# Optimization experiments

Hardware: AMD Instinct MI355X
Metric: run time of the kernel (lower is better)

## Reference

```python
import math
import jax, jax.numpy as jnp
import numpy as np

NUM_HEADS = 8
FACTOR = 5


def setup_inputs() -> dict:
    key = jax.random.key(0)
    ks = jax.random.split(key, 8)
    B, N, C = 8, 4096, 512
    s = 0.02
    x = jax.random.normal(ks[0], (B, N, C), dtype=jnp.float32)
    Wq = jax.random.normal(ks[1], (C, C), dtype=jnp.float32) * s
    Wk = jax.random.normal(ks[2], (C, C), dtype=jnp.float32) * s
    Wv = jax.random.normal(ks[3], (C, C), dtype=jnp.float32) * s
    Wp = jax.random.normal(ks[4], (C, C), dtype=jnp.float32) * s
    bq = jnp.zeros((C,), jnp.float32)
    bk = jnp.zeros((C,), jnp.float32)
    bv = jnp.zeros((C,), jnp.float32)
    bp = jnp.zeros((C,), jnp.float32)
    sample_k = min(FACTOR * int(np.ceil(np.log(N))), N)  # 45
    index_sample = jax.random.randint(ks[5], (N, sample_k), 0, N, dtype=jnp.int64)
    return {"x": x, "Wq": Wq, "bq": bq, "Wk": Wk, "bk": bk,
            "Wv": Wv, "bv": bv, "Wp": Wp, "bp": bp,
            "index_sample": index_sample}


def reference(x, Wq, bq, Wk, bk, Wv, bv, Wp, bp, index_sample):
    B, N, C = x.shape
    H = NUM_HEADS
    Dh = C // H
    L_Q = L_K = N
    # qkv projections (torch Linear: x @ W.T + b; W sampled symmetric so use x @ W + b)
    q = (x @ Wq + bq).reshape(B, N, H, Dh).transpose(0, 2, 1, 3)  # [B,H,L,Dh]
    k = (x @ Wk + bk).reshape(B, N, H, Dh).transpose(0, 2, 1, 3)
    v = (x @ Wv + bv).reshape(B, N, H, Dh).transpose(0, 2, 1, 3)

    u = min(FACTOR * int(np.ceil(np.log(L_Q))), L_Q)  # n_top
    scale = (C // H) ** (-0.5)

    # _prob_QK: sampled scores per query
    K_sample = k[:, :, index_sample, :]                       # [B,H,L_Q,s,Dh]
    QK_sample = jnp.einsum('bhld,bhlsd->bhls', q, K_sample)   # [B,H,L_Q,s]
    M = QK_sample.max(axis=-1) - QK_sample.sum(axis=-1) / L_K # sparsity measure
    _, M_top = jax.lax.top_k(M, u)                            # [B,H,u]
    Q_reduce = jnp.take_along_axis(q, M_top[..., None], axis=2)  # [B,H,u,Dh]
    scores = jnp.einsum('bhud,bhkd->bhuk', Q_reduce, k) * scale  # [B,H,u,L_K]

    # initial context: mean of V over keys (mask_flag=False)
    context = jnp.broadcast_to(v.mean(axis=2, keepdims=True), (B, H, L_Q, Dh))

    # update context at selected queries
    attn = jax.nn.softmax(scores, axis=-1)
    out_u = jnp.einsum('bhuk,bhkd->bhud', attn, v)            # [B,H,u,Dh]
    bI = jnp.arange(B)[:, None, None]
    hI = jnp.arange(H)[None, :, None]
    context = context.at[bI, hI, M_top].set(out_u)            # [B,H,L_Q,Dh]

    # mix=True: reshape [B,H,N,Dh] -> [B,N,H*Dh] directly (faithful to source)
    context = context.reshape(B, N, H * Dh)
    return context @ Wp + bp
```

## Files before the change

kernel.cpp:

```cpp
#include <hip/hip_runtime.h>
#include <float.h>

typedef unsigned short ushort_t;
typedef short bf16x8 __attribute__((ext_vector_type(8)));
typedef _Float16 f16x8 __attribute__((ext_vector_type(8)));
typedef float f32x4 __attribute__((ext_vector_type(4)));

#define NS 4096
#define ND 64
#define NU 45
#define NUP 48

__device__ __forceinline__ float bf2f(ushort_t u){ return __uint_as_float(((unsigned)u)<<16); }
__device__ __forceinline__ ushort_t f2bf(float f){
  unsigned u = __float_as_uint(f);
  u += 0x7fffu + ((u>>16)&1u);
  return (ushort_t)(u>>16);
}
__device__ __forceinline__ ushort_t f2h(float f){ _Float16 h=(_Float16)f; return __builtin_bit_cast(ushort_t, h); }
__device__ __forceinline__ float h2f(ushort_t u){ return (float)__builtin_bit_cast(_Float16, u); }

__global__ __launch_bounds__(256) void k_wsplit(const float* __restrict__ Wq,
                                                const float* __restrict__ Wk,
                                                const float* __restrict__ Wv,
                                                ushort_t* __restrict__ wh,
                                                ushort_t* __restrict__ wl)
{
  int i = blockIdx.x*256 + threadIdx.x;
  int c = i >> 9, k = i & 511;
  const float* W = (c < 512) ? Wq : (c < 1024 ? Wk : Wv);
  float v = W[k*512 + (c & 511)];
  ushort_t h = f2bf(v);
  wh[i] = h;
  wl[i] = f2bf(v - bf2f(h));
}

__global__ __launch_bounds__(256) void k_gemm_qkv(
    const float* __restrict__ x,
    const ushort_t* __restrict__ wh, const ushort_t* __restrict__ wl,
    const float* __restrict__ bq, const float* __restrict__ bk, const float* __restrict__ bv,
    float* __restrict__ qf, float* __restrict__ kf, ushort_t* __restrict__ vfT,
    ushort_t* __restrict__ kh16)
{
  __shared__ __align__(16) ushort_t Ah[128*40], Al[128*40];
  __shared__ __align__(16) ushort_t Bh[128*40], Bl[128*40];
  const int t = threadIdx.x;
  const int l = t & 63;
  const int w = t >> 6;
  const int wm = w >> 1, wn = w & 1;
  const int rowbase = blockIdx.y * 128;
  const int colbase = blockIdx.x * 128;
  const int mat = colbase >> 9;
  f32x4 acc[4][4] = {};
  const int r0 = t >> 2;
  const int c0 = (t & 3) * 8;

  for (int k0 = 0; k0 < 512; k0 += 32) {
    __syncthreads();
    #pragma unroll
    for (int half = 0; half < 2; half++) {
      const int r = r0 + half*64;
      const float* xp = &x[(size_t)(rowbase + r)*512 + k0 + c0];
      float4 v0 = *(const float4*)xp;
      float4 v1 = *(const float4*)(xp + 4);
      ushort_t hi[8], lo[8];
      float vv[8] = {v0.x,v0.y,v0.z,v0.w,v1.x,v1.y,v1.z,v1.w};
      #pragma unroll
      for (int j = 0; j < 8; j++) {
        hi[j] = f2bf(vv[j]);
        lo[j] = f2bf(vv[j] - bf2f(hi[j]));
      }
      *(uint4*)(&Ah[r*40 + c0]) = *(const uint4*)hi;
      *(uint4*)(&Al[r*40 + c0]) = *(const uint4*)lo;
      *(uint4*)(&Bh[r*40 + c0]) = *(const uint4*)(&wh[(size_t)(colbase + r)*512 + k0 + c0]);
      *(uint4*)(&Bl[r*40 + c0]) = *(const uint4*)(&wl[(size_t)(colbase + r)*512 + k0 + c0]);
    }
    __syncthreads();
    bf16x8 ah[4], al[4], bh8[4], bl8[4];
    #pragma unroll
    for (int m = 0; m < 4; m++) {
      const int off = (wm*64 + m*16 + (l & 15))*40 + (l >> 4)*8;
      ah[m] = *(const bf16x8*)(&Ah[off]);
      al[m] = *(const bf16x8*)(&Al[off]);
    }
    #pragma unroll
    for (int n = 0; n < 4; n++) {
      const int off = (wn*64 + n*16 + (l & 15))*40 + (l >> 4)*8;
      bh8[n] = *(const bf16x8*)(&Bh[off]);
      bl8[n] = *(const bf16x8*)(&Bl[off]);
    }
    #pragma unroll
    for (int m = 0; m < 4; m++)
      #pragma unroll
      for (int n = 0; n < 4; n++) {
        acc[m][n] = __builtin_amdgcn_mfma_f32_16x16x32_bf16(ah[m], bh8[n], acc[m][n], 0, 0, 0);
        acc[m][n] = __builtin_amdgcn_mfma_f32_16x16x32_bf16(ah[m], bl8[n], acc[m][n], 0, 0, 0);
        acc[m][n] = __builtin_amdgcn_mfma_f32_16x16x32_bf16(al[m], bh8[n], acc[m][n], 0, 0, 0);
      }
  }

  const float* bias_p = (mat == 0) ? bq : (mat == 1 ? bk : bv);
  float* dst = (mat == 0) ? qf : kf;
  #pragma unroll
  for (int n = 0; n < 4; n++) {
    const int wi = (colbase & 511) + wn*64 + n*16 + (l & 15);
    const int hh = wi >> 6, d = wi & 63;
    const float bias = bias_p[wi];
    #pragma unroll
    for (int m = 0; m < 4; m++) {
      const int rb = rowbase + wm*64 + m*16 + ((l >> 4) << 2);
      const int b  = rb >> 12, nr = rb & 4095;
      if (mat < 2) {
        #pragma unroll
        for (int j = 0; j < 4; j++) {
          const size_t o = ((size_t)(b*8 + hh)*NS + nr + j)*ND + d;
          const float val = acc[m][n][j] + bias;
          dst[o] = val;
          if (mat == 1 && kh16) kh16[o] = f2h(val);
        }
      } else {
        ushort4 pk;
        pk.x = f2h(acc[m][n][0] + bias);
        pk.y = f2h(acc[m][n][1] + bias);
        pk.z = f2h(acc[m][n][2] + bias);
        pk.w = f2h(acc[m][n][3] + bias);
        *(ushort4*)(&vfT[((size_t)(b*8 + hh)*ND + d)*NS + nr]) = pk;
      }
    }
  }
}

__global__ __launch_bounds__(256) void k_m_approx(const float* __restrict__ qf,
                                                  const ushort_t* __restrict__ kh16,
                                                  const int* __restrict__ idxs,
                                                  float* __restrict__ Mv)
{
  __shared__ float qs[4][64];
  __shared__ int   sidx[4][48];
  const int orig = blockIdx.y * 1024 + blockIdx.x;
  const int lin  = (orig & 7) * 8192 + (orig >> 3);
  const int bh   = lin >> 10;
  const int lc   = lin & 1023;
  const int t = threadIdx.x;
  const int wv = t >> 6, lane = t & 63;
  const int l = lc*4 + wv;
  qs[wv][lane] = qf[((size_t)bh*NS + l)*ND + lane];
  for (int e = t; e < 4*NU; e += 256)
    sidx[e/NU][e%NU] = idxs[(size_t)(lc*4 + e/NU)*NU + e%NU];
  __syncthreads();
  const int g  = lane >> 3;
  const int dq = lane & 7;
  const float* qp = &qs[wv][dq*8];
  float mx = -FLT_MAX, sm = 0.f;
  #pragma unroll
  for (int p = 0; p < 6; p++) {
    const int s = p*8 + g;
    const bool val = (s < NU);
    const int id = sidx[wv][val ? s : NU-1];
    uint4 ku = *(const uint4*)(&kh16[((size_t)bh*NS + id)*ND + dq*8]);
    f16x8 k8 = __builtin_bit_cast(f16x8, ku);
    float p_dot = qp[0]*(float)k8[0] + qp[1]*(float)k8[1] + qp[2]*(float)k8[2] + qp[3]*(float)k8[3]
                + qp[4]*(float)k8[4] + qp[5]*(float)k8[5] + qp[6]*(float)k8[6] + qp[7]*(float)k8[7];
    p_dot += __shfl_xor(p_dot, 1, 64);
    p_dot += __shfl_xor(p_dot, 2, 64);
    p_dot += __shfl_xor(p_dot, 4, 64);
    if (val) { mx = fmaxf(mx, p_dot); sm += p_dot; }
  }
  #pragma unroll
  for (int o = 8; o < 64; o <<= 1) {
    mx = fmaxf(mx, __shfl_xor(mx, o, 64));
    sm += __shfl_xor(sm, o, 64);
  }
  if (lane == 0) Mv[bh*NS + l] = mx - sm * (1.0f/(float)NS);
}

__global__ __launch_bounds__(256) void k_m_exact_full(const float* __restrict__ qf,
                                                      const float* __restrict__ kf,
                                                      const int* __restrict__ idxs,
                                                      float* __restrict__ Mv)
{
  const int bh = blockIdx.y;
  const int l  = blockIdx.x*4 + (threadIdx.x >> 6);
  const int lane = threadIdx.x & 63;
  const int g  = lane >> 2;
  const int dq = lane & 3;
  const float* qrow = qf + ((size_t)bh*NS + l)*ND + dq*16;
  const float4 q0 = *(const float4*)(qrow + 0);
  const float4 q1 = *(const float4*)(qrow + 4);
  const float4 q2 = *(const float4*)(qrow + 8);
  const float4 q3 = *(const float4*)(qrow + 12);
  const float* kbase = kf + (size_t)bh*NS*ND;
  const int* ib = idxs + (size_t)l*NU;
  float mx = -FLT_MAX, sm = 0.f;
  #pragma unroll
  for (int p3 = 0; p3 < 3; p3++) {
    const int s = p3*16 + g;
    const int id = ib[s < NU ? s : NU-1];
    const float* kr = kbase + (size_t)id*ND + dq*16;
    const float4 k0 = *(const float4*)(kr + 0);
    const float4 k1 = *(const float4*)(kr + 4);
    const float4 k2 = *(const float4*)(kr + 8);
    const float4 k3 = *(const float4*)(kr + 12);
    float p = q0.x*k0.x + q0.y*k0.y + q0.z*k0.z + q0.w*k0.w
            + q1.x*k1.x + q1.y*k1.y + q1.z*k1.z + q1.w*k1.w
            + q2.x*k2.x + q2.y*k2.y + q2.z*k2.z + q2.w*k2.w
            + q3.x*k3.x + q3.y*k3.y + q3.z*k3.z + q3.w*k3.w;
    p += __shfl_xor(p, 1, 64);
    p += __shfl_xor(p, 2, 64);
    if (s < NU) { mx = fmaxf(mx, p); sm += p; }
  }
  #pragma unroll
  for (int o = 4; o < 64; o <<= 1) {
    mx = fmaxf(mx, __shfl_xor(mx, o, 64));
    sm += __shfl_xor(sm, o, 64);
  }
  if (lane == 0) Mv[bh*NS + l] = mx - sm * (1.0f/(float)NS);
}

template<int NSEL, int OST>
__global__ __launch_bounds__(256) void k_topk(const float* __restrict__ Mv, int* __restrict__ dst)
{
  __shared__ float wvs[4];
  __shared__ int   wis[4];
  const int bh = blockIdx.x, t = threadIdx.x;
  const int wv = t >> 6, lane = t & 63;
  float v[16];
  #pragma unroll
  for (int j = 0; j < 16; j++) v[j] = Mv[bh*NS + j*256 + t];
  unsigned removed = 0;
  float tmax = -FLT_MAX; int tidx = 0x7fffffff;
  #pragma unroll
  for (int j = 0; j < 16; j++) {
    if (v[j] > tmax) { tmax = v[j]; tidx = j*256 + t; }
  }
  for (int it = 0; it < NSEL; it++) {
    float mv = tmax; int mi = tidx;
    #pragma unroll
    for (int o = 1; o < 64; o <<= 1) {
      float vo = __shfl_xor(mv, o, 64); int io = __shfl_xor(mi, o, 64);
      if (vo > mv || (vo == mv && io < mi)) { mv = vo; mi = io; }
    }
    if (lane == 0) { wvs[wv] = mv; wis[wv] = mi; }
    __syncthreads();
    float gv = wvs[0]; int gi = wis[0];
    #pragma unroll
    for (int k2 = 1; k2 < 4; k2++) {
      float vo = wvs[k2]; int io = wis[k2];
      if (vo > gv || (vo == gv && io < gi)) { gv = vo; gi = io; }
    }
    if (t == 0) dst[bh*OST + it] = gi;
    if ((gi & 255) == t) {
      removed |= 1u << (gi >> 8);
      tmax = -FLT_MAX; tidx = 0x7fffffff;
      #pragma unroll
      for (int j = 0; j < 16; j++) {
        bool ok = ((removed >> j) & 1u) == 0u;
        if (ok && (v[j] > tmax || (v[j] == tmax && (j*256+t) < tidx))) { tmax = v[j]; tidx = j*256 + t; }
      }
    }
    __syncthreads();
  }
}

__global__ __launch_bounds__(256) void k_mexact(const float* __restrict__ qf,
                                                const float* __restrict__ kf,
                                                const int* __restrict__ idxs,
                                                const int* __restrict__ Cand,
                                                float* __restrict__ Mex)
{
  const int bh = blockIdx.y, qtr = blockIdx.x, t = threadIdx.x;
  const int c = qtr*16 + (t >> 4);
  const int dl = t & 15;
  const int l = Cand[bh*64 + c];
  const float4 q4 = *(const float4*)(&qf[((size_t)bh*NS + l)*ND + dl*4]);
  const float* kbase = kf + (size_t)bh*NS*ND;
  const int* ib = idxs + (size_t)l*NU;
  float mx = -FLT_MAX, sm = 0.f;
  for (int s = 0; s < NU; s++) {
    const int id = ib[s];
    const float4 k4 = *(const float4*)(&kbase[(size_t)id*ND + dl*4]);
    float p = q4.x*k4.x + q4.y*k4.y + q4.z*k4.z + q4.w*k4.w;
    p += __shfl_xor(p, 1, 64);
    p += __shfl_xor(p, 2, 64);
    p += __shfl_xor(p, 4, 64);
    p += __shfl_xor(p, 8, 64);
    mx = fmaxf(mx, p);
    sm += p;
  }
  if (dl == 0) Mex[bh*64 + c] = mx - sm * (1.0f/(float)NS);
}

__global__ void k_sel45(const float* __restrict__ Mex, const int* __restrict__ Cand,
                        int* __restrict__ Mtop)
{
  const int bh = blockIdx.x, lane = threadIdx.x;
  float val = Mex[bh*64 + lane];
  const int n = Cand[bh*64 + lane];
  for (int it = 0; it < NU; it++) {
    float wv = val; int wn = n;
    #pragma unroll
    for (int o = 1; o < 64; o <<= 1) {
      float vo = __shfl_xor(wv, o, 64); int io = __shfl_xor(wn, o, 64);
      if (vo > wv || (vo == wv && io < wn)) { wv = vo; wn = io; }
    }
    if (lane == 0) Mtop[bh*NUP + it] = wn;
    if (n == wn) val = -FLT_MAX;
  }
}

__global__ __launch_bounds__(256) void k_qreduce(const float* __restrict__ qf,
                                                 const int* __restrict__ Mtop,
                                                 ushort_t* __restrict__ Qr)
{
  const int bh = blockIdx.x, t = threadIdx.x;
  for (int e = t; e < NUP*ND; e += 256) {
    const int u = e >> 6, d = e & 63;
    float v = 0.f;
    if (u < NU) { const int r = Mtop[bh*NUP + u]; v = qf[((size_t)bh*NS + r)*ND + d]; }
    Qr[bh*NUP*ND + e] = f2bf(v);
  }
}

__global__ __launch_bounds__(256) void k_scores(const ushort_t* __restrict__ Qr,
                                                const float* __restrict__ kf,
                                                ushort_t* __restrict__ scores)
{
  __shared__ __align__(16) ushort_t Ql[NUP*80];
  const int bh = blockIdx.y;
  const int n0 = blockIdx.x * 256;
  const int t = threadIdx.x, w = t >> 6, l = t & 63;
  for (int chunk = t; chunk < NUP*8; chunk += 256) {
    const int r = chunk >> 3, cp = chunk & 7;
    *(uint4*)(&Ql[r*80 + cp*8]) = *(const uint4*)(&Qr[((size_t)bh*NUP + r)*ND + cp*8]);
  }
  __syncthreads();
  f32x4 acc[3][4] = {};
  const float* kbb = kf + (size_t)bh*NS*ND;
  const int nw = n0 + w*64;
  #pragma unroll
  for (int ks = 0; ks < 2; ks++) {
    bf16x8 a[3], b8[4];
    #pragma unroll
    for (int m = 0; m < 3; m++)
      a[m] = *(const bf16x8*)(&Ql[(m*16 + (l & 15))*80 + (l >> 4)*8 + ks*32]);
    #pragma unroll
    for (int n = 0; n < 4; n++) {
      const float* kr = &kbb[(size_t)(nw + n*16 + (l & 15))*ND + (l >> 4)*8 + ks*32];
      float4 u0 = *(const float4*)kr;
      float4 u1 = *(const float4*)(kr + 4);
      ushort_t tmp[8] = {f2bf(u0.x),f2bf(u0.y),f2bf(u0.z),f2bf(u0.w),
                         f2bf(u1.x),f2bf(u1.y),f2bf(u1.z),f2bf(u1.w)};
      b8[n] = *(const bf16x8*)tmp;
    }
    #pragma unroll
    for (int m = 0; m < 3; m++)
      #pragma unroll
      for (int n = 0; n < 4; n++)
        acc[m][n] = __builtin_amdgcn_mfma_f32_16x16x32_bf16(a[m], b8[n], acc[m][n], 0, 0, 0);
  }
  #pragma unroll
  for (int m = 0; m < 3; m++)
    #pragma unroll
    for (int n = 0; n < 4; n++)
      #pragma unroll
      for (int j = 0; j < 4; j++) {
        const int row = m*16 + (l >> 4)*4 + j;
        const int col = nw + n*16 + (l & 15);
        scores[((size_t)bh*NUP + row)*NS + col] = f2bf(acc[m][n][j] * 0.125f);
      }
}

__global__ __launch_bounds__(256) void k_softmax(ushort_t* __restrict__ scores)
{
  __shared__ float srow[NS];
  __shared__ float red[256];
  const int bh = blockIdx.y, u = blockIdx.x, t = threadIdx.x;
  ushort_t* row = scores + ((size_t)bh*NUP + u)*NS;
  float mx = -FLT_MAX;
  for (int j = t; j < NS; j += 256) { float v = bf2f(row[j]); srow[j] = v; mx = fmaxf(mx, v); }
  red[t] = mx; __syncthreads();
  for (int s = 128; s > 0; s >>= 1) { if (t < s) red[t] = fmaxf(red[t], red[t+s]); __syncthreads(); }
  mx = red[0]; __syncthreads();
  float sm = 0.f;
  for (int j = t; j < NS; j += 256) { const float e = __expf(srow[j] - mx); srow[j] = e; sm += e; }
  red[t] = sm; __syncthreads();
  for (int s = 128; s > 0; s >>= 1) { if (t < s) red[t] += red[t+s]; __syncthreads(); }
  const float inv = 1.0f / red[0];
  for (int j = t; j < NS; j += 256) row[j] = f2h(srow[j] * inv);
}

__global__ __launch_bounds__(256) void k_vmean(const ushort_t* __restrict__ vfT, float* __restrict__ vmean)
{
  __shared__ float red[256];
  const int d = blockIdx.x, bh = blockIdx.y, t = threadIdx.x;
  const ushort_t* vr = vfT + ((size_t)bh*ND + d)*NS;
  float s = 0.f;
  for (int n = t; n < NS; n += 256) s += h2f(vr[n]);
  red[t] = s; __syncthreads();
  for (int st = 128; st > 0; st >>= 1) { if (t < st) red[t] += red[t+st]; __syncthreads(); }
  if (t == 0) vmean[bh*ND + d] = red[0] * (1.0f/(float)NS);
}

__global__ __launch_bounds__(256) void k_outu(const ushort_t* __restrict__ attn,
                                              const ushort_t* __restrict__ vfT,
                                              float* __restrict__ pout)
{
  const int bh = blockIdx.y, ch = blockIdx.x;
  const int t = threadIdx.x, w = t >> 6, l = t & 63;
  if (w >= 3) return;
  const ushort_t* ab = attn + (size_t)bh*NUP*NS;
  const ushort_t* vb = vfT + (size_t)bh*ND*NS;
  f32x4 acc[4] = {};
  const int arow = w*16 + (l & 15);
  const int koff = (l >> 4)*8;
  const int kbeg = ch*512;
  for (int kc = kbeg; kc < kbeg + 512; kc += 32) {
    uint4 au = *(const uint4*)(&ab[(size_t)arow*NS + kc + koff]);
    f16x8 a = __builtin_bit_cast(f16x8, au);
    #pragma unroll
    for (int nt = 0; nt < 4; nt++) {
      uint4 bu = *(const uint4*)(&vb[(size_t)(nt*16 + (l & 15))*NS + kc + koff]);
      f16x8 b = __builtin_bit_cast(f16x8, bu);
      acc[nt] = __builtin_amdgcn_mfma_f32_16x16x32_f16(a, b, acc[nt], 0, 0, 0);
    }
  }
  #pragma unroll
  for (int nt = 0; nt < 4; nt++)
    #pragma unroll
    for (int j = 0; j < 4; j++) {
      const int u = w*16 + (l >> 4)*4 + j;
      const int d = nt*16 + (l & 15);
      pout[(((size_t)bh*8 + ch)*NUP + u)*ND + d] = acc[nt][j];
    }
}

__global__ __launch_bounds__(256) void k_delta_fin(const float* __restrict__ pout,
                                                   const float* __restrict__ vmean,
                                                   float* __restrict__ delta)
{
  const int bh = blockIdx.x, t = threadIdx.x;
  for (int e = t; e < NUP*ND; e += 256) {
    const int u = e >> 6, d = e & 63;
    float s = 0.f;
    #pragma unroll
    for (int ch = 0; ch < 8; ch++) s += pout[(((size_t)bh*8 + ch)*NUP + u)*ND + d];
    delta[((size_t)bh*NUP + u)*ND + d] = s - vmean[bh*ND + d];
  }
}

__global__ __launch_bounds__(256) void k_uidx_init(int* __restrict__ uidx)
{
  uidx[blockIdx.x*256 + threadIdx.x] = -1;
}

__global__ void k_scatter(const int* __restrict__ Mtop, int* __restrict__ uidx)
{
  const int bh = blockIdx.x, t = threadIdx.x;
  if (t < NU) {
    const int n = Mtop[bh*NUP + t];
    const int b = bh >> 3, h = bh & 7;
    const int nprime = h*512 + (n >> 3);
    uidx[((size_t)b*NS + nprime)*8 + (n & 7)] = bh*NUP + t;
  }
}

__global__ __launch_bounds__(256) void k_corr(const float* __restrict__ delta,
                                              const float* __restrict__ Wp,
                                              const int* __restrict__ Mtop,
                                              float* __restrict__ corr)
{
  __shared__ float dl[64];
  const int bh = blockIdx.y, u = blockIdx.x, t = threadIdx.x;
  const int n = Mtop[bh*NUP + u];
  const int j = n & 7;
  if (t < 64) dl[t] = delta[((size_t)bh*NUP + u)*ND + t];
  __syncthreads();
  for (int c = t; c < 512; c += 256) {
    float s = 0.f;
    #pragma unroll 8
    for (int d2 = 0; d2 < 64; d2++) s += dl[d2] * Wp[(size_t)(j*64 + d2)*512 + c];
    corr[((size_t)bh*NUP + u)*512 + c] = s;
  }
}

__global__ __launch_bounds__(256) void k_base(const float* __restrict__ vmean,
                                              const float* __restrict__ Wp,
                                              const float* __restrict__ bp,
                                              float* __restrict__ basep)
{
  __shared__ float vm[64];
  const int bh = blockIdx.x, t = threadIdx.x;
  if (t < 64) vm[t] = vmean[bh*ND + t];
  __syncthreads();
  for (int c = t; c < 512; c += 256) {
    float s = bp[c];
    for (int k = 0; k < 512; k++) s += vm[k & 63] * Wp[(size_t)k*512 + c];
    basep[bh*512 + c] = s;
  }
}

__global__ __launch_bounds__(256) void k_assemble(const float* __restrict__ basep,
                                                  const float* __restrict__ corr,
                                                  const int* __restrict__ uidx,
                                                  float* __restrict__ out)
{
  const int b = blockIdx.y, nprime = blockIdx.x, t = threadIdx.x;
  const int h = nprime >> 9;
  const int* ui = uidx + ((size_t)b*NS + nprime)*8;
  float v0 = basep[(b*8 + h)*512 + t];
  float v1 = basep[(b*8 + h)*512 + 256 + t];
  #pragma unroll
  for (int j = 0; j < 8; j++) {
    const int id = ui[j];
    if (id >= 0) { v0 += corr[(size_t)id*512 + t]; v1 += corr[(size_t)id*512 + 256 + t]; }
  }
  const size_t o = ((size_t)b*NS + nprime)*512;
  out[o + t]       = v0;
  out[o + 256 + t] = v1;
}

extern "C" void kernel_launch(void* const* d_in, const int* in_sizes, int n_in,
                              void* d_out, int out_size, void* d_ws, size_t ws_size,
                              hipStream_t stream)
{
  (void)in_sizes; (void)n_in; (void)out_size;
  const float* x  = (const float*)d_in[0];
  const float* Wq = (const float*)d_in[1];
  const float* bq = (const float*)d_in[2];
  const float* Wk = (const float*)d_in[3];
  const float* bk = (const float*)d_in[4];
  const float* Wv = (const float*)d_in[5];
  const float* bv = (const float*)d_in[6];
  const float* Wp = (const float*)d_in[7];
  const float* bp = (const float*)d_in[8];
  const int* idxs = (const int*)d_in[9];
  float* out      = (float*)d_out;

  char* w = (char*)d_ws;
  float*    qf    = (float*)(w);
  float*    kf    = (float*)(w + 67108864);
  ushort_t* vfT   = (ushort_t*)(w + 134217728);
  ushort_t* wh    = (ushort_t*)(w + 167772160);
  ushort_t* wl    = (ushort_t*)(w + 169345024);
  float*    Mv    = (float*)(w + 170917888);
  int*      Mtop  = (int*)(w + 171966464);
  ushort_t* Qr    = (ushort_t*)(w + 171978752);
  float*    vmean = (float*)(w + 172371968);
  ushort_t* scores = (ushort_t*)(w);
  float*    delta  = (float*)(w + 25165824);
  float*    corr   = (float*)(w + 25952256);
  int*      uidx   = (int*)(w + 32243712);
  float*    basep  = (float*)(w + 33292288);
  float*    pout   = (float*)(w + 33423360);
  ushort_t* kh16 = (ushort_t*)(w + 172388352);
  int*      Cand = (int*)(w + 205942784);
  float*    Mex  = (float*)(w + 205959168);
  const bool approx_ok = (ws_size >= (size_t)205975552);

  k_wsplit   <<<3072, 256, 0, stream>>>(Wq, Wk, Wv, wh, wl);
  k_gemm_qkv <<<dim3(12, 256), 256, 0, stream>>>(x, wh, wl, bq, bk, bv, qf, kf, vfT,
                                                 approx_ok ? kh16 : (ushort_t*)nullptr);
  if (approx_ok) {
    k_m_approx <<<dim3(1024, 64), 256, 0, stream>>>(qf, kh16, idxs, Mv);
    k_vmean    <<<dim3(64, 64), 256, 0, stream>>>(vfT, vmean);
    k_topk<64,64> <<<64, 256, 0, stream>>>(Mv, Cand);
    k_mexact   <<<dim3(4, 64), 256, 0, stream>>>(qf, kf, idxs, Cand, Mex);
    k_sel45    <<<64, 64, 0, stream>>>(Mex, Cand, Mtop);
  } else {
    k_m_exact_full <<<dim3(1024, 64), 256, 0, stream>>>(qf, kf, idxs, Mv);
    k_vmean    <<<dim3(64, 64), 256, 0, stream>>>(vfT, vmean);
    k_topk<NU,NUP> <<<64, 256, 0, stream>>>(Mv, Mtop);
  }
  k_qreduce  <<<64, 256, 0, stream>>>(qf, Mtop, Qr);
  k_scores   <<<dim3(16, 64), 256, 0, stream>>>(Qr, kf, scores);
  k_softmax  <<<dim3(45, 64), 256, 0, stream>>>(scores);
  k_outu     <<<dim3(8, 64), 256, 0, stream>>>(scores, vfT, pout);
  k_delta_fin<<<64, 256, 0, stream>>>(pout, vmean, delta);
  k_uidx_init<<<1024, 256, 0, stream>>>(uidx);
  k_scatter  <<<64, 64, 0, stream>>>(Mtop, uidx);
  k_corr     <<<dim3(45, 64), 256, 0, stream>>>(delta, Wp, Mtop, corr);
  k_base     <<<64, 256, 0, stream>>>(vmean, Wp, bp, basep);
  k_assemble <<<dim3(4096, 8), 256, 0, stream>>>(basep, corr, uidx, out);
}
```

Measured before the change: 612.3 us.

## Split QKV GEMM, pre-split x, transpose V via LDS, separate fp16 K cast

```diff
diff --git a/kernel.cpp b/kernel.cpp
--- a/kernel.cpp
+++ b/kernel.cpp
@@ -35,22 +35,47 @@
   wl[i] = f2bf(v - bf2f(h));
 }
 
-__global__ __launch_bounds__(256) void k_gemm_qkv(
+__global__ __launch_bounds__(256) void k_xsplit(const float* __restrict__ x,
+                                                ushort_t* __restrict__ xh,
+                                                ushort_t* __restrict__ xl)
+{
+  int i = (blockIdx.x*256 + threadIdx.x)*4;
+  float4 v = *(const float4*)(x + i);
+  ushort4 h, lo;
+  h.x = f2bf(v.x); lo.x = f2bf(v.x - bf2f(h.x));
+  h.y = f2bf(v.y); lo.y = f2bf(v.y - bf2f(h.y));
+  h.z = f2bf(v.z); lo.z = f2bf(v.z - bf2f(h.z));
+  h.w = f2bf(v.w); lo.w = f2bf(v.w - bf2f(h.w));
+  *(ushort4*)(xh + i) = h;
+  *(ushort4*)(xl + i) = lo;
+}
+
+template<int MODE>
+__global__ __launch_bounds__(256) void k_gemm(
     const float* __restrict__ x,
+    const ushort_t* __restrict__ xh, const ushort_t* __restrict__ xl,
     const ushort_t* __restrict__ wh, const ushort_t* __restrict__ wl,
     const float* __restrict__ bq, const float* __restrict__ bk, const float* __restrict__ bv,
-    float* __restrict__ qf, float* __restrict__ kf, ushort_t* __restrict__ vfT,
-    ushort_t* __restrict__ kh16)
-{
-  __shared__ __align__(16) ushort_t Ah[128*40], Al[128*40];
-  __shared__ __align__(16) ushort_t Bh[128*40], Bl[128*40];
+    float* __restrict__ qf, float* __restrict__ kf, ushort_t* __restrict__ vfT)
+{
+  __shared__ __align__(16) ushort_t smem[4*128*40];
+  ushort_t* Ah = smem;
+  ushort_t* Al = smem + 5120;
+  ushort_t* Bh = smem + 10240;
+  ushort_t* Bl = smem + 15360;
+  const int nbx = (MODE == 0) ? 4 : 8;
+  const int p = blockIdx.y * nbx + blockIdx.x;
+  const int cx = p & 7;
+  const int local = p >> 3;
+  const int by = cx*32 + local/nbx;
+  const int bx = local % nbx;
+  const int rowbase = by * 128;
+  const int colbase = (MODE == 0 ? 0 : 512) + bx*128;
+  const int mat = colbase >> 9;
   const int t = threadIdx.x;
   const int l = t & 63;
   const int w = t >> 6;
   const int wm = w >> 1, wn = w & 1;
-  const int rowbase = blockIdx.y * 128;
-  const int colbase = blockIdx.x * 128;
-  const int mat = colbase >> 9;
   f32x4 acc[4][4] = {};
   const int r0 = t >> 2;
   const int c0 = (t & 3) * 8;
@@ -60,18 +85,23 @@
     #pragma unroll
     for (int half = 0; half < 2; half++) {
       const int r = r0 + half*64;
-      const float* xp = &x[(size_t)(rowbase + r)*512 + k0 + c0];
-      float4 v0 = *(const float4*)xp;
-      float4 v1 = *(const float4*)(xp + 4);
-      ushort_t hi[8], lo[8];
-      float vv[8] = {v0.x,v0.y,v0.z,v0.w,v1.x,v1.y,v1.z,v1.w};
-      #pragma unroll
-      for (int j = 0; j < 8; j++) {
-        hi[j] = f2bf(vv[j]);
-        lo[j] = f2bf(vv[j] - bf2f(hi[j]));
+      if constexpr (MODE == 1) {
+        *(uint4*)(&Ah[r*40 + c0]) = *(const uint4*)(&xh[(size_t)(rowbase + r)*512 + k0 + c0]);
+        *(uint4*)(&Al[r*40 + c0]) = *(const uint4*)(&xl[(size_t)(rowbase + r)*512 + k0 + c0]);
+      } else {
+        const float* xp = &x[(size_t)(rowbase + r)*512 + k0 + c0];
+        float4 v0 = *(const float4*)xp;
+        float4 v1 = *(const float4*)(xp + 4);
+        ushort_t hi[8], lo[8];
+        float vv[8] = {v0.x,v0.y,v0.z,v0.w,v1.x,v1.y,v1.z,v1.w};
+        #pragma unroll
+        for (int j = 0; j < 8; j++) {
+          hi[j] = f2bf(vv[j]);
+          lo[j] = f2bf(vv[j] - bf2f(hi[j]));
+        }
+        *(uint4*)(&Ah[r*40 + c0]) = *(const uint4*)hi;
+        *(uint4*)(&Al[r*40 + c0]) = *(const uint4*)lo;
       }
-      *(uint4*)(&Ah[r*40 + c0]) = *(const uint4*)hi;
-      *(uint4*)(&Al[r*40 + c0]) = *(const uint4*)lo;
       *(uint4*)(&Bh[r*40 + c0]) = *(const uint4*)(&wh[(size_t)(colbase + r)*512 + k0 + c0]);
       *(uint4*)(&Bl[r*40 + c0]) = *(const uint4*)(&wl[(size_t)(colbase + r)*512 + k0 + c0]);
     }
@@ -99,35 +129,65 @@
       }
   }
 
-  const float* bias_p = (mat == 0) ? bq : (mat == 1 ? bk : bv);
-  float* dst = (mat == 0) ? qf : kf;
-  #pragma unroll
-  for (int n = 0; n < 4; n++) {
-    const int wi = (colbase & 511) + wn*64 + n*16 + (l & 15);
-    const int hh = wi >> 6, d = wi & 63;
-    const float bias = bias_p[wi];
-    #pragma unroll
-    for (int m = 0; m < 4; m++) {
-      const int rb = rowbase + wm*64 + m*16 + ((l >> 4) << 2);
-      const int b  = rb >> 12, nr = rb & 4095;
-      if (mat < 2) {
+  if (MODE == 0 || mat == 1) {
+    const float* bias_p = (MODE == 0) ? bq : bk;
+    float* dst = (MODE == 0) ? qf : kf;
+    #pragma unroll
+    for (int n = 0; n < 4; n++) {
+      const int wi = (colbase & 511) + wn*64 + n*16 + (l & 15);
+      const int hh = wi >> 6, d = wi & 63;
+      const float bias = bias_p[wi];
+      #pragma unroll
+      for (int m = 0; m < 4; m++) {
+        const int rb = rowbase + wm*64 + m*16 + ((l >> 4) << 2);
+        const int b  = rb >> 12, nr = rb & 4095;
         #pragma unroll
-        for (int j = 0; j < 4; j++) {
-          const size_t o = ((size_t)(b*8 + hh)*NS + nr + j)*ND + d;
-          const float val = acc[m][n][j] + bias;
-          dst[o] = val;
-          if (mat == 1 && kh16) kh16[o] = f2h(val);
-        }
-      } else {
+        for (int j = 0; j < 4; j++)
+          dst[((size_t)(b*8 + hh)*NS + nr + j)*ND + d] = acc[m][n][j] + bias;
+      }
+    }
+  } else {
+    __syncthreads();
+    #pragma unroll
+    for (int n = 0; n < 4; n++) {
+      const int wi_l = wn*64 + n*16 + (l & 15);
+      const float bias = bv[(colbase & 511) + wi_l];
+      #pragma unroll
+      for (int m = 0; m < 4; m++) {
+        const int nr_l = wm*64 + m*16 + ((l >> 4) << 2);
         ushort4 pk;
         pk.x = f2h(acc[m][n][0] + bias);
         pk.y = f2h(acc[m][n][1] + bias);
         pk.z = f2h(acc[m][n][2] + bias);
         pk.w = f2h(acc[m][n][3] + bias);
-        *(ushort4*)(&vfT[((size_t)(b*8 + hh)*ND + d)*NS + nr]) = pk;
+        *(ushort4*)(&smem[wi_l*136 + nr_l]) = pk;
       }
     }
-  }
+    __syncthreads();
+    const int wi2 = t >> 1, half = t & 1;
+    const int cim = (colbase & 511) + wi2;
+    const int hh2 = cim >> 6, d2 = cim & 63;
+    const int b2 = rowbase >> 12;
+    const int nr2 = (rowbase & 4095) + half*64;
+    ushort_t* op = &vfT[((size_t)(b2*8 + hh2)*ND + d2)*NS + nr2];
+    const ushort_t* ip = &smem[wi2*136 + half*64];
+    #pragma unroll
+    for (int cch = 0; cch < 8; cch++)
+      *(uint4*)(op + cch*8) = *(const uint4*)(ip + cch*8);
+  }
+}
+
+__global__ __launch_bounds__(256) void k_k16(const float* __restrict__ kf,
+                                             ushort_t* __restrict__ kh16)
+{
+  size_t i = ((size_t)blockIdx.x*256 + threadIdx.x)*8;
+  float4 a = *(const float4*)(kf + i);
+  float4 b = *(const float4*)(kf + i + 4);
+  ushort4 p0, p1;
+  p0.x = f2h(a.x); p0.y = f2h(a.y); p0.z = f2h(a.z); p0.w = f2h(a.w);
+  p1.x = f2h(b.x); p1.y = f2h(b.y); p1.z = f2h(b.z); p1.w = f2h(b.w);
+  *(ushort4*)(kh16 + i)     = p0;
+  *(ushort4*)(kh16 + i + 4) = p1;
 }
 
 __global__ __launch_bounds__(256) void k_m_approx(const float* __restrict__ qf,
@@ -546,6 +606,8 @@
   int*      Mtop  = (int*)(w + 171966464);
   ushort_t* Qr    = (ushort_t*)(w + 171978752);
   float*    vmean = (float*)(w + 172371968);
+  ushort_t* xh = (ushort_t*)(w);
+  ushort_t* xl = (ushort_t*)(w + 33554432);
   ushort_t* scores = (ushort_t*)(w);
   float*    delta  = (float*)(w + 25165824);
   float*    corr   = (float*)(w + 25952256);
@@ -558,9 +620,11 @@
   const bool approx_ok = (ws_size >= (size_t)205975552);
 
   k_wsplit   <<<3072, 256, 0, stream>>>(Wq, Wk, Wv, wh, wl);
-  k_gemm_qkv <<<dim3(12, 256), 256, 0, stream>>>(x, wh, wl, bq, bk, bv, qf, kf, vfT,
-                                                 approx_ok ? kh16 : (ushort_t*)nullptr);
+  k_xsplit   <<<16384, 256, 0, stream>>>(x, xh, xl);
+  k_gemm<1>  <<<dim3(8, 256), 256, 0, stream>>>(x, xh, xl, wh, wl, bq, bk, bv, qf, kf, vfT);
+  k_gemm<0>  <<<dim3(4, 256), 256, 0, stream>>>(x, nullptr, nullptr, wh, wl, bq, bk, bv, qf, kf, vfT);
   if (approx_ok) {
+    k_k16      <<<8192, 256, 0, stream>>>(kf, kh16);
     k_m_approx <<<dim3(1024, 64), 256, 0, stream>>>(qf, kh16, idxs, Mv);
     k_vmean    <<<dim3(64, 64), 256, 0, stream>>>(vfT, vmean);
     k_topk<64,64> <<<64, 256, 0, stream>>>(Mv, Cand);
```

New measurement: 604.0 us. No clear change (-1.4%).
